# Kernel tuning notes

Hardware: AMD Instinct MI355X
Metric: run time of the kernel (lower is better)

## Reference

```python
import jax, jax.numpy as jnp
import numpy as np

MICRO_BATCHES = 4
NUM_EXPERTS = 8  # world_size=1 -> num_local_experts = 8
EPS = 1e-5


def setup_inputs() -> dict:
    key = jax.random.key(0)
    ks = jax.random.split(key, 8)
    B, S, D = 8, 2048, 1024
    E, F = NUM_EXPERTS, 4 * D
    x = jax.random.normal(ks[0], (B, S, D), dtype=jnp.float32)
    gamma = jnp.ones((D,), jnp.float32)
    beta = jnp.zeros((D,), jnp.float32)
    gate_w = jax.random.normal(ks[1], (E, D), jnp.float32) * (1.0 / np.sqrt(D))
    w1 = jax.random.normal(ks[2], (E, D, F), jnp.float32) * (1.0 / np.sqrt(D))
    b1 = jnp.zeros((E, F), jnp.float32)
    w2 = jax.random.normal(ks[3], (E, F, D), jnp.float32) * (1.0 / np.sqrt(F))
    b2 = jnp.zeros((E, D), jnp.float32)
    return {"x": x, "gamma": gamma, "beta": beta, "gate_w": gate_w,
            "w1": w1, "b1": b1, "w2": w2, "b2": b2}


def reference(x, gamma, beta, gate_w, w1, b1, w2, b2):
    B, S, D = x.shape
    E = w1.shape[0]
    # micro-batch chunking along batch dim (chunk(MICRO_BATCHES, dim=0))
    xf = x.reshape(MICRO_BATCHES, -1, D)            # [MB, T, D], T = B/MB * S
    T = xf.shape[1]
    # residual (gated_input) is the pre-LN flat input
    # moe_norm: LayerNorm over last dim, biased variance, eps=1e-5
    mu = jnp.mean(xf, axis=-1, keepdims=True)
    var = jnp.mean(jnp.square(xf - mu), axis=-1, keepdims=True)
    xn = (xf - mu) * jax.lax.rsqrt(var + EPS) * gamma + beta  # [MB, T, D]
    # gate logits + topk are computed in the source but discarded
    _logits = jnp.einsum('mtd,ed->mte', xn, gate_w)
    _ = jax.lax.top_k(_logits, 2)
    # dispatch/combine are identity for world_size=1; tokens split round-robin
    # into num_local_experts contiguous chunks per micro-batch
    tpe = T // E
    xe = xn.reshape(MICRO_BATCHES, E, tpe, D)       # [MB, E, tpe, D]
    h = jax.nn.gelu(jnp.einsum('metd,edf->metf', xe, w1) + b1[None, :, None, :],
                    approximate=False)
    y = jnp.einsum('metf,efd->metd', h, w2) + b2[None, :, None, :]
    out = xf + y.reshape(MICRO_BATCHES, T, D)       # residual add
    return out.reshape(B, S, D)
```

## Files before the change

### kernel.cpp

```cpp
#include <hip/hip_runtime.h>
#include <stdint.h>
#include <math.h>

typedef unsigned short ushort_t;
typedef __attribute__((ext_vector_type(8))) short bf16x8;
typedef __attribute__((ext_vector_type(4))) float f32x4;

#define SLOT 32768

__device__ __forceinline__ ushort_t f2bf(float f) {
  union { float f; unsigned u; } cv; cv.f = f;
  unsigned r = cv.u + 0x7fffu + ((cv.u >> 16) & 1u);
  return (ushort_t)(r >> 16);
}

__device__ __forceinline__ void gl_lds16(const void* g, void* l) {
  typedef __attribute__((address_space(1))) const char gchar;
  typedef __attribute__((address_space(3))) char lchar;
  __builtin_amdgcn_global_load_lds((gchar*)g, (lchar*)l, 16, 0, 0);
}

__device__ __forceinline__ f32x4 MFMA(bf16x8 a, bf16x8 b, f32x4 c) {
  return __builtin_amdgcn_mfma_f32_16x16x32_bf16(a, b, c, 0, 0, 0);
}

__global__ __launch_bounds__(256) void ln_kernel(const float* __restrict__ x,
                                                 const float* __restrict__ gamma,
                                                 const float* __restrict__ beta,
                                                 ushort_t* __restrict__ xn) {
  const int row = blockIdx.x;
  const int t = threadIdx.x;
  const float4 v = ((const float4*)(x + (size_t)row * 1024))[t];
  float s  = v.x + v.y + v.z + v.w;
  float ss = v.x * v.x + v.y * v.y + v.z * v.z + v.w * v.w;
#pragma unroll
  for (int o = 32; o >= 1; o >>= 1) {
    s  += __shfl_xor(s, o);
    ss += __shfl_xor(ss, o);
  }
  __shared__ float red[10];
  const int wave = t >> 6, lane = t & 63;
  if (lane == 0) { red[wave] = s; red[4 + wave] = ss; }
  __syncthreads();
  if (t == 0) {
    float S  = red[0] + red[1] + red[2] + red[3];
    float SS = red[4] + red[5] + red[6] + red[7];
    float mu  = S * (1.0f / 1024.0f);
    float var = SS * (1.0f / 1024.0f) - mu * mu;
    red[8] = mu;
    red[9] = rsqrtf(var + 1e-5f);
  }
  __syncthreads();
  const float mu = red[8], rs = red[9];
  const float4 g = ((const float4*)gamma)[t];
  const float4 b = ((const float4*)beta)[t];
  ushort4 o;
  o.x = f2bf((v.x - mu) * rs * g.x + b.x);
  o.y = f2bf((v.y - mu) * rs * g.y + b.y);
  o.z = f2bf((v.z - mu) * rs * g.z + b.z);
  o.w = f2bf((v.w - mu) * rs * g.w + b.w);
  ((ushort4*)(xn + (size_t)row * 1024))[t] = o;
}

__global__ __launch_bounds__(256) void transpose_cast(const float* __restrict__ in,
                                                      ushort_t* __restrict__ out,
                                                      int R, int C) {
  __shared__ float tile[32][33];
  const int e = blockIdx.z;
  const float* src = in + (size_t)e * R * C;
  ushort_t* dst = out + (size_t)e * R * C;
  const int c0 = blockIdx.x * 32, r0 = blockIdx.y * 32;
  const int tx = threadIdx.x, ty = threadIdx.y;
#pragma unroll
  for (int j = 0; j < 32; j += 8)
    tile[ty + j][tx] = src[(size_t)(r0 + ty + j) * C + c0 + tx];
  __syncthreads();
#pragma unroll
  for (int j = 0; j < 32; j += 8)
    dst[(size_t)(c0 + ty + j) * R + r0 + tx] = f2bf(tile[tx][ty + j]);
}


__device__ __forceinline__ void stage_half(const ushort_t* gsrc, int lda,
                                           char* half_base, int kt, int tid) {
  const int rr = tid >> 2;
  const int gs = (tid & 3) ^ ((tid >> 3) & 3);
  gl_lds16(gsrc + (size_t)rr * lda + kt + gs * 8, half_base + (tid >> 6) * 1024);
}

template <int VM, bool STG>
__device__ __forceinline__ void tile_body(char* smem, int T,
                                          const ushort_t* gA, const ushort_t* gB,
                                          int lda, int a_off, int b_off, int tid,
                                          f32x4 (&acc)[8][4]) {
  const char* slot = smem + (T & 3) * SLOT;
  char* nslot = smem + ((T + 3) & 3) * SLOT;
  const int kt3 = (T + 3) * 32;
  bf16x8 a[4], b[4];
#pragma unroll
  for (int ni = 0; ni < 4; ni++) b[ni] = *(const bf16x8*)(slot + b_off + ni * 1024);
#pragma unroll
  for (int mi = 0; mi < 4; mi++) a[mi] = *(const bf16x8*)(slot + a_off + mi * 1024);
  if (STG) {
    stage_half(gA, lda, nslot, kt3, tid);
    stage_half(gA + (size_t)128 * lda, lda, nslot + 8192, kt3, tid);
  }
  __builtin_amdgcn_s_barrier();
  asm volatile("s_waitcnt lgkmcnt(0)" ::: "memory");
  __builtin_amdgcn_s_setprio(1);
#pragma unroll
  for (int mi = 0; mi < 4; mi++)
#pragma unroll
    for (int ni = 0; ni < 4; ni++)
      acc[mi][ni] = MFMA(a[mi], b[ni], acc[mi][ni]);
  __builtin_amdgcn_s_setprio(0);
  __builtin_amdgcn_s_barrier();
#pragma unroll
  for (int mi = 0; mi < 4; mi++) a[mi] = *(const bf16x8*)(slot + a_off + (mi + 4) * 1024);
  if (STG) {
    stage_half(gB, lda, nslot + 16384, kt3, tid);
    stage_half(gB + (size_t)128 * lda, lda, nslot + 24576, kt3, tid);
  }
  if (VM == 8)      asm volatile("s_waitcnt vmcnt(8) lgkmcnt(0)" ::: "memory");
  else if (VM == 4) asm volatile("s_waitcnt vmcnt(4) lgkmcnt(0)" ::: "memory");
  else if (VM == 0) asm volatile("s_waitcnt vmcnt(0) lgkmcnt(0)" ::: "memory");
  else              asm volatile("s_waitcnt lgkmcnt(0)" ::: "memory");
  __builtin_amdgcn_s_barrier();
  __builtin_amdgcn_s_setprio(1);
#pragma unroll
  for (int mi = 0; mi < 4; mi++)
#pragma unroll
    for (int ni = 0; ni < 4; ni++)
      acc[mi + 4][ni] = MFMA(a[mi], b[ni], acc[mi + 4][ni]);
  __builtin_amdgcn_s_setprio(0);
  __builtin_amdgcn_s_barrier();
}

template <int EPI, int LDA, int LDC, int KTOT>
__global__ __launch_bounds__(512, 2) void gemm256(const ushort_t* __restrict__ A,
                                                  const ushort_t* __restrict__ Bw,
                                                  const float* __restrict__ bias,
                                                  const float* __restrict__ resid,
                                                  ushort_t* __restrict__ Hout,
                                                  float* __restrict__ Fout) {
  extern __shared__ char smem[];
  const int tid = threadIdx.x;
  const int wave = tid >> 6, lane = tid & 63;

  const int bid = blockIdx.x;
  const int c = bid & 7, l = bid >> 3;
  const int tm = c * 8 + (l & 7);
  const int tn = l >> 3;
  const int row0 = tm * 256;
  const int col0 = tn * 256;
  const int e = (row0 >> 9) & 7;

  const ushort_t* gA = A + (size_t)row0 * LDA;
  const ushort_t* gB = Bw + ((size_t)e * LDC + col0) * LDA;

  const int NT = KTOT / 32;

  const int wm = wave >> 2, wn = wave & 3;
  const int l15 = lane & 15, g = lane >> 4;
  const int sw = ((g ^ ((lane >> 1) & 3)) << 4);
  const int a_off = wm * 8192 + l15 * 64 + sw;
  const int b_off = 16384 + (wn >> 1) * 8192 + (wn & 1) * 4096 + l15 * 64 + sw;

  f32x4 acc[8][4] = {};

#pragma unroll
  for (int T = 0; T < 3; ++T) {
    char* s = smem + T * SLOT;
    stage_half(gA, LDA, s, T * 32, tid);
    stage_half(gA + (size_t)128 * LDA, LDA, s + 8192, T * 32, tid);
    stage_half(gB, LDA, s + 16384, T * 32, tid);
    stage_half(gB + (size_t)128 * LDA, LDA, s + 24576, T * 32, tid);
  }
  asm volatile("s_waitcnt vmcnt(8)" ::: "memory");
  __builtin_amdgcn_s_barrier();

#pragma unroll 4
  for (int T = 0; T < NT - 3; ++T)
    tile_body<8, true>(smem, T, gA, gB, LDA, a_off, b_off, tid, acc);
  tile_body<4, false>(smem, NT - 3, gA, gB, LDA, a_off, b_off, tid, acc);
  tile_body<0, false>(smem, NT - 2, gA, gB, LDA, a_off, b_off, tid, acc);
  tile_body<-1, false>(smem, NT - 1, gA, gB, LDA, a_off, b_off, tid, acc);

  const int rbase = row0 + wm * 128 + g * 4;
  const int cbase = col0 + wn * 64 + l15;
  const float* bp = bias + e * LDC;
#pragma unroll
  for (int ni = 0; ni < 4; ni++) {
    const int n = cbase + ni * 16;
    const float bv = bp[n];
#pragma unroll
    for (int mi = 0; mi < 8; mi++) {
#pragma unroll
      for (int r = 0; r < 4; r++) {
        const int row = rbase + mi * 16 + r;
        float v = acc[mi][ni][r] + bv;
        if (EPI == 0) {
          float v2 = v * v;
          float cc = fmaf(0.044715f, v2, 1.0f);
          float xa = -2.3022078f * v * cc;
          float u  = exp2f(xa);
          float o  = __fdividef(v, 1.0f + u);
          Hout[(size_t)row * LDC + n] = (ushort_t)f2bf(o);
        } else {
          const size_t idx = (size_t)row * LDC + n;
          Fout[idx] = resid[idx] + v;
        }
      }
    }
  }
}

extern "C" void kernel_launch(void* const* d_in, const int* in_sizes, int n_in,
                              void* d_out, int out_size, void* d_ws, size_t ws_size,
                              hipStream_t stream) {
  const float* x     = (const float*)d_in[0];
  const float* gamma = (const float*)d_in[1];
  const float* beta  = (const float*)d_in[2];
  const float* w1    = (const float*)d_in[4];
  const float* b1    = (const float*)d_in[5];
  const float* w2    = (const float*)d_in[6];
  const float* b2    = (const float*)d_in[7];
  float* out = (float*)d_out;

  char* ws = (char*)d_ws;
  ushort_t* xn  = (ushort_t*)ws;
  ushort_t* w1t = (ushort_t*)(ws + 33554432);
  ushort_t* w2t = (ushort_t*)(ws + 33554432 + 67108864);
  ushort_t* h   = (ushort_t*)(ws + 33554432 + 2 * 67108864);

  hipFuncSetAttribute(reinterpret_cast<const void*>(&gemm256<0, 1024, 4096, 1024>),
                      hipFuncAttributeMaxDynamicSharedMemorySize, 131072);
  hipFuncSetAttribute(reinterpret_cast<const void*>(&gemm256<1, 4096, 1024, 4096>),
                      hipFuncAttributeMaxDynamicSharedMemorySize, 131072);

  ln_kernel<<<16384, 256, 0, stream>>>(x, gamma, beta, xn);
  transpose_cast<<<dim3(128, 32, 8), dim3(32, 8), 0, stream>>>(w1, w1t, 1024, 4096);
  transpose_cast<<<dim3(32, 128, 8), dim3(32, 8), 0, stream>>>(w2, w2t, 4096, 1024);

  gemm256<0, 1024, 4096, 1024><<<dim3(1024), 512, 131072, stream>>>(xn, w1t, b1, nullptr, h, nullptr);
  gemm256<1, 4096, 1024, 4096><<<dim3(256), 512, 131072, stream>>>(h, w2t, b2, x, nullptr, out);
}
```

Before: 463.8 us.

## Double-buffer LDS fragment reads across tiles and stage epilogue through LDS

Restructures the GEMM main loop so the A/B fragment reads for the next K-tile are issued during the second MFMA half of the current tile. B fragments ping-pong between two register sets, and the vmcnt waits and barrier placement are adjusted. The epilogue now writes results into LDS with a padded stride and then emits coalesced vectorized global stores (ushort4/float4), with vectorized residual loads. This aims to hide LDS read latency behind MFMA work and to replace scattered scalar stores, at the cost of more registers and extra barriers.

After: 424.0 us. 1.09x faster.

```diff
diff --git a/kernel.cpp b/kernel.cpp
--- a/kernel.cpp
+++ b/kernel.cpp
@@ -7,6 +7,7 @@
 typedef __attribute__((ext_vector_type(4))) float f32x4;
 
 #define SLOT 32768
+#define EPI_STRIDE 1032
 
 __device__ __forceinline__ ushort_t f2bf(float f) {
   union { float f; unsigned u; } cv; cv.f = f;
@@ -88,51 +89,56 @@
   gl_lds16(gsrc + (size_t)rr * lda + kt + gs * 8, half_base + (tid >> 6) * 1024);
 }
 
-template <int VM, bool STG>
+template <int BASE>
+__device__ __forceinline__ void mfma16(const bf16x8 (&a)[4], const bf16x8 (&b)[4],
+                                       f32x4 (&acc)[8][4]) {
+  __builtin_amdgcn_s_setprio(1);
+#pragma unroll
+  for (int mi = 0; mi < 4; mi++)
+#pragma unroll
+    for (int ni = 0; ni < 4; ni++)
+      acc[BASE + mi][ni] = MFMA(a[mi], b[ni], acc[BASE + mi][ni]);
+  __builtin_amdgcn_s_setprio(0);
+}
+
+template <int VM, bool STG, bool LAST>
 __device__ __forceinline__ void tile_body(char* smem, int T,
                                           const ushort_t* gA, const ushort_t* gB,
                                           int lda, int a_off, int b_off, int tid,
+                                          bf16x8 (&bA0)[4], bf16x8 (&bA1)[4],
+                                          bf16x8 (&bBc)[4], bf16x8 (&bBn)[4],
                                           f32x4 (&acc)[8][4]) {
   const char* slot = smem + (T & 3) * SLOT;
-  char* nslot = smem + ((T + 3) & 3) * SLOT;
+  char* nstg = smem + ((T + 3) & 3) * SLOT;
   const int kt3 = (T + 3) * 32;
-  bf16x8 a[4], b[4];
-#pragma unroll
-  for (int ni = 0; ni < 4; ni++) b[ni] = *(const bf16x8*)(slot + b_off + ni * 1024);
-#pragma unroll
-  for (int mi = 0; mi < 4; mi++) a[mi] = *(const bf16x8*)(slot + a_off + mi * 1024);
+#pragma unroll
+  for (int mi = 0; mi < 4; mi++) bA1[mi] = *(const bf16x8*)(slot + a_off + (mi + 4) * 1024);
   if (STG) {
-    stage_half(gA, lda, nslot, kt3, tid);
-    stage_half(gA + (size_t)128 * lda, lda, nslot + 8192, kt3, tid);
-  }
-  __builtin_amdgcn_s_barrier();
-  asm volatile("s_waitcnt lgkmcnt(0)" ::: "memory");
-  __builtin_amdgcn_s_setprio(1);
-#pragma unroll
-  for (int mi = 0; mi < 4; mi++)
-#pragma unroll
-    for (int ni = 0; ni < 4; ni++)
-      acc[mi][ni] = MFMA(a[mi], b[ni], acc[mi][ni]);
-  __builtin_amdgcn_s_setprio(0);
-  __builtin_amdgcn_s_barrier();
-#pragma unroll
-  for (int mi = 0; mi < 4; mi++) a[mi] = *(const bf16x8*)(slot + a_off + (mi + 4) * 1024);
-  if (STG) {
-    stage_half(gB, lda, nslot + 16384, kt3, tid);
-    stage_half(gB + (size_t)128 * lda, lda, nslot + 24576, kt3, tid);
-  }
-  if (VM == 8)      asm volatile("s_waitcnt vmcnt(8) lgkmcnt(0)" ::: "memory");
-  else if (VM == 4) asm volatile("s_waitcnt vmcnt(4) lgkmcnt(0)" ::: "memory");
-  else if (VM == 0) asm volatile("s_waitcnt vmcnt(0) lgkmcnt(0)" ::: "memory");
-  else              asm volatile("s_waitcnt lgkmcnt(0)" ::: "memory");
-  __builtin_amdgcn_s_barrier();
-  __builtin_amdgcn_s_setprio(1);
-#pragma unroll
-  for (int mi = 0; mi < 4; mi++)
-#pragma unroll
-    for (int ni = 0; ni < 4; ni++)
-      acc[mi + 4][ni] = MFMA(a[mi], b[ni], acc[mi + 4][ni]);
-  __builtin_amdgcn_s_setprio(0);
+    stage_half(gA, lda, nstg, kt3, tid);
+    stage_half(gA + (size_t)128 * lda, lda, nstg + 8192, kt3, tid);
+  }
+  __builtin_amdgcn_sched_barrier(0);
+  __builtin_amdgcn_s_barrier();
+  __builtin_amdgcn_sched_barrier(0);
+  mfma16<0>(bA0, bBc, acc);
+  __builtin_amdgcn_s_barrier();
+  if (VM == 6)      asm volatile("s_waitcnt vmcnt(6)" ::: "memory");
+  else if (VM == 4) asm volatile("s_waitcnt vmcnt(4)" ::: "memory");
+  else if (VM == 0) asm volatile("s_waitcnt vmcnt(0)" ::: "memory");
+  __builtin_amdgcn_s_barrier();
+  if (!LAST) {
+    const char* nslot = smem + ((T + 1) & 3) * SLOT;
+#pragma unroll
+    for (int ni = 0; ni < 4; ni++) bBn[ni] = *(const bf16x8*)(nslot + b_off + ni * 1024);
+#pragma unroll
+    for (int mi = 0; mi < 4; mi++) bA0[mi] = *(const bf16x8*)(nslot + a_off + mi * 1024);
+    if (STG) {
+      stage_half(gB, lda, nstg + 16384, kt3, tid);
+      stage_half(gB + (size_t)128 * lda, lda, nstg + 24576, kt3, tid);
+    }
+  }
+  __builtin_amdgcn_sched_barrier(0);
+  mfma16<4>(bA1, bBc, acc);
   __builtin_amdgcn_s_barrier();
 }
 
@@ -167,6 +173,7 @@
   const int b_off = 16384 + (wn >> 1) * 8192 + (wn & 1) * 4096 + l15 * 64 + sw;
 
   f32x4 acc[8][4] = {};
+  bf16x8 bA0[4], bA1[4], bB0[4], bB1[4];
 
 #pragma unroll
   for (int T = 0; T < 3; ++T) {
@@ -178,40 +185,70 @@
   }
   asm volatile("s_waitcnt vmcnt(8)" ::: "memory");
   __builtin_amdgcn_s_barrier();
-
-#pragma unroll 4
-  for (int T = 0; T < NT - 3; ++T)
-    tile_body<8, true>(smem, T, gA, gB, LDA, a_off, b_off, tid, acc);
-  tile_body<4, false>(smem, NT - 3, gA, gB, LDA, a_off, b_off, tid, acc);
-  tile_body<0, false>(smem, NT - 2, gA, gB, LDA, a_off, b_off, tid, acc);
-  tile_body<-1, false>(smem, NT - 1, gA, gB, LDA, a_off, b_off, tid, acc);
-
-  const int rbase = row0 + wm * 128 + g * 4;
-  const int cbase = col0 + wn * 64 + l15;
-  const float* bp = bias + e * LDC;
-#pragma unroll
-  for (int ni = 0; ni < 4; ni++) {
-    const int n = cbase + ni * 16;
-    const float bv = bp[n];
-#pragma unroll
-    for (int mi = 0; mi < 8; mi++) {
-#pragma unroll
-      for (int r = 0; r < 4; r++) {
-        const int row = rbase + mi * 16 + r;
-        float v = acc[mi][ni][r] + bv;
-        if (EPI == 0) {
-          float v2 = v * v;
-          float cc = fmaf(0.044715f, v2, 1.0f);
-          float xa = -2.3022078f * v * cc;
-          float u  = exp2f(xa);
-          float o  = __fdividef(v, 1.0f + u);
-          Hout[(size_t)row * LDC + n] = (ushort_t)f2bf(o);
-        } else {
-          const size_t idx = (size_t)row * LDC + n;
-          Fout[idx] = resid[idx] + v;
+#pragma unroll
+  for (int ni = 0; ni < 4; ni++) bB0[ni] = *(const bf16x8*)(smem + b_off + ni * 1024);
+#pragma unroll
+  for (int mi = 0; mi < 4; mi++) bA0[mi] = *(const bf16x8*)(smem + a_off + mi * 1024);
+
+  for (int T = 0; T < NT - 4; T += 2) {
+    tile_body<6, true, false>(smem, T,     gA, gB, LDA, a_off, b_off, tid, bA0, bA1, bB0, bB1, acc);
+    tile_body<6, true, false>(smem, T + 1, gA, gB, LDA, a_off, b_off, tid, bA0, bA1, bB1, bB0, acc);
+  }
+  tile_body<6, true,  false>(smem, NT - 4, gA, gB, LDA, a_off, b_off, tid, bA0, bA1, bB0, bB1, acc);
+  tile_body<4, false, false>(smem, NT - 3, gA, gB, LDA, a_off, b_off, tid, bA0, bA1, bB1, bB0, acc);
+  tile_body<0, false, false>(smem, NT - 2, gA, gB, LDA, a_off, b_off, tid, bA0, bA1, bB0, bB1, acc);
+  tile_body<-1, false, true>(smem, NT - 1, gA, gB, LDA, a_off, b_off, tid, bA0, bA1, bB1, bB0, acc);
+
+  __syncthreads();
+
+  float bv[4];
+#pragma unroll
+  for (int ni = 0; ni < 4; ni++)
+    bv[ni] = bias[e * LDC + col0 + wn * 64 + ni * 16 + l15];
+
+#pragma unroll
+  for (int r = 0; r < 4; ++r) {
+#pragma unroll
+    for (int mh = 0; mh < 2; ++mh) {
+      const int mi = 2 * r + mh;
+      const int lrow = wm * 32 + mh * 16 + g * 4;
+#pragma unroll
+      for (int ni = 0; ni < 4; ++ni) {
+        const int colb = (wn * 64 + ni * 16 + l15) * 4;
+#pragma unroll
+        for (int rr = 0; rr < 4; ++rr) {
+          float v = acc[mi][ni][rr] + bv[ni];
+          if (EPI == 0) {
+            float v2 = v * v;
+            float cc = fmaf(0.044715f, v2, 1.0f);
+            float u  = exp2f(-2.3022078f * v * cc);
+            v = __fdividef(v, 1.0f + u);
+          }
+          *(float*)(smem + (size_t)(lrow + rr) * EPI_STRIDE + colb) = v;
         }
       }
     }
+    __syncthreads();
+#pragma unroll
+    for (int i = 0; i < 8; ++i) {
+      const int chunk = i * 512 + tid;
+      const int lr = chunk >> 6;
+      const int cb = (chunk & 63) * 16;
+      const float4 v4 = *(const float4*)(smem + (size_t)lr * EPI_STRIDE + cb);
+      const int grow = row0 + (lr < 32 ? r * 32 + lr : 128 + r * 32 + (lr - 32));
+      const int gcol = col0 + (chunk & 63) * 4;
+      if (EPI == 0) {
+        ushort4 o;
+        o.x = f2bf(v4.x); o.y = f2bf(v4.y); o.z = f2bf(v4.z); o.w = f2bf(v4.w);
+        *(ushort4*)(&Hout[(size_t)grow * LDC + gcol]) = o;
+      } else {
+        const float4 rs = *(const float4*)(&resid[(size_t)grow * LDC + gcol]);
+        float4 o;
+        o.x = v4.x + rs.x; o.y = v4.y + rs.y; o.z = v4.z + rs.z; o.w = v4.w + rs.w;
+        *(float4*)(&Fout[(size_t)grow * LDC + gcol]) = o;
+      }
+    }
+    __syncthreads();
   }
 }
 
```
